# Kernel optimization log

Hardware: AMD Instinct MI355X
Metric: run time of the kernel (lower is better)

Reference implementation:

```python
import jax, jax.numpy as jnp
import numpy as np

THRESH = 0.5  # sklearn Binarizer(threshold=0.5): strictly greater -> 1
SMOOTH = 1  # declared in original but unused in returned values


def setup_inputs() -> dict:
    key = jax.random.key(0)
    k1, k2 = jax.random.split(key)
    shape = (32, 1, 1024, 1024)
    inp = jax.random.uniform(k1, shape, dtype=jnp.float32)
    tgt = jax.random.uniform(k2, shape, dtype=jnp.float32)
    return {"input": inp, "target": tgt}


def reference(input, target):
    N = target.shape[0]
    input_flat = input.reshape(N, -1)
    target_flat = target.reshape(N, -1)
    # original detaches + binarizes on CPU; math = hard threshold, no grad
    input_bin = (jax.lax.stop_gradient(input_flat) > THRESH).astype(input_flat.dtype)
    intersection = input_bin * target_flat
    loss1 = 2 * intersection.sum()
    loss2 = input_bin.sum() + target_flat.sum()
    return (loss1, loss2)
```

## Files before the change

### kernel.cpp

```cpp
#include <hip/hip_runtime.h>


__global__ __launch_bounds__(256) void dice_loss_kernel(
    const float* __restrict__ inp, const float* __restrict__ tgt,
    float* __restrict__ out, long long n4)
{
    const float4* __restrict__ in4 = (const float4*)inp;
    const float4* __restrict__ tg4 = (const float4*)tgt;

    long long idx    = (long long)blockIdx.x * blockDim.x + threadIdx.x;
    long long stride = (long long)gridDim.x * blockDim.x;

    float s_inter = 0.f;
    float s_bin   = 0.f;
    float s_tgt   = 0.f;

    for (long long i = idx; i < n4; i += stride) {
        float4 a = in4[i];
        float4 b = tg4[i];
        float b0 = (a.x > 0.5f) ? 1.f : 0.f;
        float b1 = (a.y > 0.5f) ? 1.f : 0.f;
        float b2 = (a.z > 0.5f) ? 1.f : 0.f;
        float b3 = (a.w > 0.5f) ? 1.f : 0.f;
        s_bin   += (b0 + b1) + (b2 + b3);
        s_tgt   += (b.x + b.y) + (b.z + b.w);
        s_inter += (b0 * b.x + b1 * b.y) + (b2 * b.z + b3 * b.w);
    }

    #pragma unroll
    for (int off = 32; off > 0; off >>= 1) {
        s_inter += __shfl_down(s_inter, off, 64);
        s_bin   += __shfl_down(s_bin,   off, 64);
        s_tgt   += __shfl_down(s_tgt,   off, 64);
    }

    __shared__ float red[3][4];
    int wave = threadIdx.x >> 6;
    int lane = threadIdx.x & 63;
    if (lane == 0) {
        red[0][wave] = s_inter;
        red[1][wave] = s_bin;
        red[2][wave] = s_tgt;
    }
    __syncthreads();
    if (threadIdx.x == 0) {
        float ti = (red[0][0] + red[0][1]) + (red[0][2] + red[0][3]);
        float tb = (red[1][0] + red[1][1]) + (red[1][2] + red[1][3]);
        float tt = (red[2][0] + red[2][1]) + (red[2][2] + red[2][3]);
        atomicAdd(&out[0], 2.f * ti);
        atomicAdd(&out[1], tb + tt);
    }
}

extern "C" void kernel_launch(void* const* d_in, const int* in_sizes, int n_in,
                              void* d_out, int out_size, void* d_ws, size_t ws_size,
                              hipStream_t stream) {
    const float* inp = (const float*)d_in[0];
    const float* tgt = (const float*)d_in[1];
    float* out = (float*)d_out;

    long long n  = (long long)in_sizes[0];
    long long n4 = n / 4;

    hipMemsetAsync(d_out, 0, 2 * sizeof(float), stream);

    const int block = 256;
    const int grid  = 2048;
    dice_loss_kernel<<<grid, block, 0, stream>>>(inp, tgt, out, n4);
}
```

Before: 301.6 us.

## Split dice reduction into bitmask pass, target pass and final reduce

Replaces the single grid-stride kernel with three kernels. The first binarizes the input into a bitmask in workspace and writes per-block counts, the second streams the target with the mask to compute per-block sums, and the third reduces the partials deterministically without atomics. Each pass now streams one large array with fixed per-block tiles, but the mask adds an extra write and read plus two extra launches.

```diff
diff --git a/kernel.cpp b/kernel.cpp
--- a/kernel.cpp
+++ b/kernel.cpp
@@ -1,54 +1,141 @@
 #include <hip/hip_runtime.h>
 
 
-__global__ __launch_bounds__(256) void dice_loss_kernel(
-    const float* __restrict__ inp, const float* __restrict__ tgt,
-    float* __restrict__ out, long long n4)
+#define T1 256
+#define BLK_E 16384LL
+
+__global__ __launch_bounds__(T1) void dice_mask_kernel(
+    const float* __restrict__ inp, unsigned char* __restrict__ mask,
+    float* __restrict__ pbin, long long n)
 {
     const float4* __restrict__ in4 = (const float4*)inp;
+    const int wave = threadIdx.x >> 6;
+    const int lane = threadIdx.x & 63;
+    const long long wv_e = (long long)blockIdx.x * BLK_E + (long long)wave * 4096;
+
+    float s_bin = 0.f;
+
+    if (wv_e + 4096 <= n) {
+        const long long f4 = (wv_e >> 2) + (long long)lane * 2;
+        const long long mb = (wv_e >> 3) + lane;
+        #pragma unroll
+        for (int k = 0; k < 8; ++k) {
+            float4 a0 = in4[f4 + k * 128];
+            float4 a1 = in4[f4 + k * 128 + 1];
+            unsigned m = (a0.x > 0.5f ? 1u   : 0u) | (a0.y > 0.5f ? 2u   : 0u)
+                       | (a0.z > 0.5f ? 4u   : 0u) | (a0.w > 0.5f ? 8u   : 0u)
+                       | (a1.x > 0.5f ? 16u  : 0u) | (a1.y > 0.5f ? 32u  : 0u)
+                       | (a1.z > 0.5f ? 64u  : 0u) | (a1.w > 0.5f ? 128u : 0u);
+            mask[mb + (long long)k * 64] = (unsigned char)m;
+            s_bin += (float)__popc(m);
+        }
+    } else {
+        for (int k = 0; k < 8; ++k) {
+            long long e0 = wv_e + (long long)k * 512 + (long long)lane * 8;
+            if (e0 < n) {
+                unsigned m = 0;
+                for (int j = 0; j < 8; ++j) {
+                    long long e = e0 + j;
+                    if (e < n && inp[e] > 0.5f) m |= (1u << j);
+                }
+                mask[e0 >> 3] = (unsigned char)m;
+                s_bin += (float)__popc(m);
+            }
+        }
+    }
+
+    #pragma unroll
+    for (int off = 32; off > 0; off >>= 1) s_bin += __shfl_down(s_bin, off, 64);
+    __shared__ float red[4];
+    if (lane == 0) red[wave] = s_bin;
+    __syncthreads();
+    if (threadIdx.x == 0)
+        pbin[blockIdx.x] = (red[0] + red[1]) + (red[2] + red[3]);
+}
+
+__global__ __launch_bounds__(T1) void dice_tgt_kernel(
+    const float* __restrict__ tgt, const unsigned char* __restrict__ mask,
+    float* __restrict__ pint, float* __restrict__ ptgt, long long n)
+{
     const float4* __restrict__ tg4 = (const float4*)tgt;
+    const int wave = threadIdx.x >> 6;
+    const int lane = threadIdx.x & 63;
+    const long long wv_e = (long long)blockIdx.x * BLK_E + (long long)wave * 4096;
 
-    long long idx    = (long long)blockIdx.x * blockDim.x + threadIdx.x;
-    long long stride = (long long)gridDim.x * blockDim.x;
+    float s_inter = 0.f, s_tgt = 0.f;
 
-    float s_inter = 0.f;
-    float s_bin   = 0.f;
-    float s_tgt   = 0.f;
-
-    for (long long i = idx; i < n4; i += stride) {
-        float4 a = in4[i];
-        float4 b = tg4[i];
-        float b0 = (a.x > 0.5f) ? 1.f : 0.f;
-        float b1 = (a.y > 0.5f) ? 1.f : 0.f;
-        float b2 = (a.z > 0.5f) ? 1.f : 0.f;
-        float b3 = (a.w > 0.5f) ? 1.f : 0.f;
-        s_bin   += (b0 + b1) + (b2 + b3);
-        s_tgt   += (b.x + b.y) + (b.z + b.w);
-        s_inter += (b0 * b.x + b1 * b.y) + (b2 * b.z + b3 * b.w);
+    if (wv_e + 4096 <= n) {
+        const long long f4 = (wv_e >> 2) + (long long)lane * 2;
+        const long long mb = (wv_e >> 3) + lane;
+        #pragma unroll
+        for (int k = 0; k < 8; ++k) {
+            float4 b0 = tg4[f4 + k * 128];
+            float4 b1 = tg4[f4 + k * 128 + 1];
+            unsigned m = mask[mb + (long long)k * 64];
+            s_tgt   += (b0.x + b0.y) + (b0.z + b0.w)
+                     + (b1.x + b1.y) + (b1.z + b1.w);
+            s_inter += ((m & 1u   ? b0.x : 0.f) + (m & 2u   ? b0.y : 0.f))
+                     + ((m & 4u   ? b0.z : 0.f) + (m & 8u   ? b0.w : 0.f))
+                     + ((m & 16u  ? b1.x : 0.f) + (m & 32u  ? b1.y : 0.f))
+                     + ((m & 64u  ? b1.z : 0.f) + (m & 128u ? b1.w : 0.f));
+        }
+    } else {
+        for (int k = 0; k < 8; ++k) {
+            long long e0 = wv_e + (long long)k * 512 + (long long)lane * 8;
+            if (e0 < n) {
+                unsigned m = mask[e0 >> 3];
+                for (int j = 0; j < 8; ++j) {
+                    long long e = e0 + j;
+                    if (e < n) {
+                        float v = tgt[e];
+                        s_tgt += v;
+                        if (m & (1u << j)) s_inter += v;
+                    }
+                }
+            }
+        }
     }
 
     #pragma unroll
     for (int off = 32; off > 0; off >>= 1) {
         s_inter += __shfl_down(s_inter, off, 64);
-        s_bin   += __shfl_down(s_bin,   off, 64);
         s_tgt   += __shfl_down(s_tgt,   off, 64);
     }
+    __shared__ float red[2][4];
+    if (lane == 0) { red[0][wave] = s_inter; red[1][wave] = s_tgt; }
+    __syncthreads();
+    if (threadIdx.x == 0) {
+        pint[blockIdx.x] = (red[0][0] + red[0][1]) + (red[0][2] + red[0][3]);
+        ptgt[blockIdx.x] = (red[1][0] + red[1][1]) + (red[1][2] + red[1][3]);
+    }
+}
 
+__global__ __launch_bounds__(T1) void dice_final_kernel(
+    const float* __restrict__ pp, float* __restrict__ out, int P)
+{
+    float s_bin = 0.f, s_int = 0.f, s_tgt = 0.f;
+    for (int i = threadIdx.x; i < P; i += T1) {
+        s_bin += pp[i];
+        s_int += pp[P + i];
+        s_tgt += pp[2 * P + i];
+    }
+    #pragma unroll
+    for (int off = 32; off > 0; off >>= 1) {
+        s_bin += __shfl_down(s_bin, off, 64);
+        s_int += __shfl_down(s_int, off, 64);
+        s_tgt += __shfl_down(s_tgt, off, 64);
+    }
     __shared__ float red[3][4];
     int wave = threadIdx.x >> 6;
     int lane = threadIdx.x & 63;
-    if (lane == 0) {
-        red[0][wave] = s_inter;
-        red[1][wave] = s_bin;
-        red[2][wave] = s_tgt;
-    }
+    if (lane == 0) { red[0][wave] = s_bin; red[1][wave] = s_int; red[2][wave] = s_tgt; }
     __syncthreads();
     if (threadIdx.x == 0) {
-        float ti = (red[0][0] + red[0][1]) + (red[0][2] + red[0][3]);
-        float tb = (red[1][0] + red[1][1]) + (red[1][2] + red[1][3]);
+        float tb = (red[0][0] + red[0][1]) + (red[0][2] + red[0][3]);
+        float ti = (red[1][0] + red[1][1]) + (red[1][2] + red[1][3]);
         float tt = (red[2][0] + red[2][1]) + (red[2][2] + red[2][3]);
-        atomicAdd(&out[0], 2.f * ti);
-        atomicAdd(&out[1], tb + tt);
+        out[0] = 2.f * ti;
+        out[1] = tb + tt;
     }
 }
 
@@ -59,12 +146,14 @@
     const float* tgt = (const float*)d_in[1];
     float* out = (float*)d_out;
 
-    long long n  = (long long)in_sizes[0];
-    long long n4 = n / 4;
+    long long n = (long long)in_sizes[0];
+    unsigned char* mask = (unsigned char*)d_ws;
+    long long mask_bytes = (n + 7) >> 3;
+    float* pp = (float*)((char*)d_ws + ((mask_bytes + 255) & ~255LL));
 
-    hipMemsetAsync(d_out, 0, 2 * sizeof(float), stream);
+    const int grid1 = (int)((n + BLK_E - 1) / BLK_E);
 
-    const int block = 256;
-    const int grid  = 2048;
-    dice_loss_kernel<<<grid, block, 0, stream>>>(inp, tgt, out, n4);
+    dice_mask_kernel<<<grid1, T1, 0, stream>>>(inp, mask, pp, n);
+    dice_tgt_kernel<<<grid1, T1, 0, stream>>>(tgt, mask, pp + grid1, pp + 2 * grid1, n);
+    dice_final_kernel<<<1, T1, 0, stream>>>(pp, out, grid1);
 }
```

After: 286.9 us. -4.9%, faster.
